# Kernel tuning notes

Hardware: AMD Instinct MI355X
Metric: run time of the kernel (lower is better)

The kernel has to match this reference:

```python
import jax, jax.numpy as jnp
import numpy as np

N_NODES = 50000
N_EDGES = 400000
H, D = 4, 32  # num_heads, per-head dim
NEG_SLOPE = 0.1


def setup_inputs() -> dict:
    key = jax.random.key(0)
    ks = jax.random.split(key, 12)
    inp = {
        'features': jax.random.normal(ks[0], (N_NODES, 256), jnp.float32) * 0.1,
        'src': jax.random.randint(ks[1], (N_EDGES,), 0, N_NODES, jnp.int32),
        'dst': jax.random.randint(ks[2], (N_EDGES,), 0, N_NODES, jnp.int32),
        'w': jax.random.uniform(ks[3], (N_EDGES,), jnp.float32),
        'W1': jax.random.normal(ks[4], (256, 128), jnp.float32) * 0.05,
        'al1': jax.random.normal(ks[5], (H, D), jnp.float32) * 0.1,
        'ar1': jax.random.normal(ks[6], (H, D), jnp.float32) * 0.1,
        'W2': jax.random.normal(ks[7], (128, 128), jnp.float32) * 0.05,
        'al2': jax.random.normal(ks[8], (H, D), jnp.float32) * 0.1,
        'ar2': jax.random.normal(ks[9], (H, D), jnp.float32) * 0.1,
        'Wout': jax.random.normal(ks[10], (256, 128), jnp.float32) * 0.05,
        'bout': jnp.zeros((128,), jnp.float32),
    }
    return inp


def _gat_layer(x, W, al, ar, src, dst, w):
    # x: [N, in_dim] -> ft: [N, H, D]
    ft = (x @ W).reshape(-1, H, D)
    el = jnp.einsum('nhd,hd->nh', ft, al)  # left attention logits per node
    er = jnp.einsum('nhd,hd->nh', ft, ar)
    # edge logits: leaky_relu(el[src] + er[dst]), then edge-weight scaling
    e = jax.nn.leaky_relu(el[src] + er[dst], negative_slope=NEG_SLOPE)  # [E, H]
    e = w[:, None] * e
    # segment softmax over incoming edges of each destination node
    m = jax.ops.segment_max(e, dst, num_segments=N_NODES)  # [N, H]
    a = jnp.exp(e - m[dst])
    s = jax.ops.segment_sum(a, dst, num_segments=N_NODES)
    a = a / s[dst]  # [E, H]
    # weighted scatter-sum aggregation: rst[dst] += a * ft[src]
    msg = ft[src] * a[:, :, None]  # [E, H, D]
    rst = jax.ops.segment_sum(msg, dst, num_segments=N_NODES)  # [N, H, D]
    # activation=relu, then concat heads (contiguous -> reshape)
    return jax.nn.relu(rst).reshape(-1, H * D)


def reference(features, src, dst, w, W1, al1, ar1, W2, al2, ar2, Wout, bout):
    x1 = _gat_layer(features, W1, al1, ar1, src, dst, w)  # [N, 128]
    x2 = _gat_layer(x1, W2, al2, ar2, src, dst, w)        # [N, 128]
    h = jnp.concatenate([x1, x2], axis=-1)                # [N, 256]
    return h @ Wout + bout                                # [N, 128]
```

## Files before the change

kernel.cpp:

```cpp
#include <hip/hip_runtime.h>
#include <math.h>

#define NHEAD 4
#define HDIM 32
#define NEG_SLOPE 0.1f

typedef unsigned short u16;
typedef unsigned int u32;
typedef _Float16 f16;
typedef f16 f16x2 __attribute__((ext_vector_type(2)));
typedef f16 f16x4 __attribute__((ext_vector_type(4)));
typedef f16 f16x8 __attribute__((ext_vector_type(8)));
typedef float f32x4 __attribute__((ext_vector_type(4)));

#define GLLDS16(g, l) __builtin_amdgcn_global_load_lds( \
    (const __attribute__((address_space(1))) void*)(g), \
    (__attribute__((address_space(3))) void*)(l), 16, 0, 0)


__device__ __forceinline__ void cast_panel(const float* __restrict__ W,
                                           const float* __restrict__ al,
                                           const float* __restrict__ ar,
                                           u16* __restrict__ bp, int t, int NC) {
    int per_kt = NC * 16;
    int kt = t / per_kt;
    int rem = t - kt * per_kt;
    int n = rem >> 4;
    int kkp = rem & 15;
    int k = kt * 32 + kkp * 2;
    float v0 = 0.f, v1 = 0.f;
    if (n < 128) {
        v0 = W[(size_t)k * 128 + n];
        v1 = W[(size_t)(k + 1) * 128 + n];
    } else if (n < 136) {
        const float* av = (n < 132) ? al : ar;
        int h = (n < 132) ? (n - 128) : (n - 132);
        float s0 = 0.f, s1 = 0.f;
        for (int d = 0; d < 32; d++) {
            float a = av[h * 32 + d];
            s0 += W[(size_t)k * 128 + h * 32 + d] * a;
            s1 += W[(size_t)(k + 1) * 128 + h * 32 + d] * a;
        }
        v0 = s0; v1 = s1;
    }
    f16x2 p;
    p.x = (f16)v0; p.y = (f16)v1;
    *(f16x2*)&((u32*)bp)[t] = p;
}

__global__ void histcast_k(const int* __restrict__ dst, int* __restrict__ cnt, int E,
                           const float* __restrict__ W1, const float* __restrict__ al1,
                           const float* __restrict__ ar1, u16* __restrict__ b1,
                           const float* __restrict__ W2, const float* __restrict__ al2,
                           const float* __restrict__ ar2, u16* __restrict__ b2,
                           const float* __restrict__ W3, u16* __restrict__ b3) {
    int t = blockIdx.x * 256 + threadIdx.x;
    if (t < E) atomicAdd(&cnt[dst[t]], 1);
    if (t < 18432) cast_panel(W1, al1, ar1, b1, t, 144);
    else if (t < 27648) cast_panel(W2, al2, ar2, b2, t - 18432, 144);
    else if (t < 44032) cast_panel(W3, nullptr, nullptr, b3, t - 27648, 128);
}


__global__ void assign_k(const int* __restrict__ cnt, int* __restrict__ start,
                         int* __restrict__ ctr, int N) {
    __shared__ int s[256];
    __shared__ int base;
    int t = threadIdx.x;
    int i = blockIdx.x * 256 + t;
    int v = (i < N) ? cnt[i] : 0;
    s[t] = v;
    __syncthreads();
    int incl = v;
    for (int off = 1; off < 256; off <<= 1) {
        int add = (t >= off) ? s[t - off] : 0;
        __syncthreads();
        incl += add;
        s[t] = incl;
        __syncthreads();
    }
    if (t == 255) base = atomicAdd(ctr, incl);
    __syncthreads();
    if (i < N) start[i] = base + incl - v;
}

__global__ void scatter_k(const int* __restrict__ src, const int* __restrict__ dst,
                          const float* __restrict__ w, const int* __restrict__ start,
                          int* __restrict__ fill, int2* __restrict__ edge_s, int E) {
    int e = blockIdx.x * 256 + threadIdx.x;
    if (e >= E) return;
    int d = dst[e];
    int p = atomicAdd(&fill[d], 1);
    edge_s[start[d] + p] = make_int2(src[e], __float_as_int(w[e]));
}


template <int NT>
__global__ __launch_bounds__(256) void gemm_h_k(
        const void* __restrict__ Av, int a_is_f16, int lda,
        const u16* __restrict__ Bp,
        const float* __restrict__ bias, float* __restrict__ Cf,
        u16* __restrict__ Ch, float* __restrict__ el, float* __restrict__ er,
        int M, int K) {
    __shared__ u16 As[2048];
    __shared__ u16 Bs[NT * 512];
    int tid = threadIdx.x;
    int w = tid >> 6, lane = tid & 63;
    int row0 = blockIdx.x * 64;
    int mrow = lane & 15;
    int koff = (lane >> 4) * 8;

    f32x4 acc[NT];
#pragma unroll
    for (int nt = 0; nt < NT; nt++) acc[nt] = (f32x4){0.f, 0.f, 0.f, 0.f};

    for (int k0 = 0; k0 < K; k0 += 32) {
        int kt = k0 >> 5;
#pragma unroll
        for (int i = 0; i < (NT * 64 + 255) / 256; i++) {
            int c = tid + i * 256;
            if (c < NT * 64)
                GLLDS16(Bp + (size_t)kt * (NT * 512) + (size_t)c * 8, &Bs[c * 8]);
        }
        if (a_is_f16) {
            const u16* Ah = (const u16*)Av;
            int c = tid;
            int r = c >> 2, kk = (c & 3) << 3;
            GLLDS16(Ah + (size_t)(row0 + r) * lda + k0 + kk, &As[c * 8]);
        } else {
            const float* Af = (const float*)Av;
#pragma unroll
            for (int i = 0; i < 2; i++) {
                int flat = tid + i * 256;
                int r = flat >> 3, c4 = flat & 7;
                int row = min(row0 + r, M - 1);
                float4 v = *(const float4*)&Af[(size_t)row * lda + k0 + c4 * 4];
                f16x4 p;
                p.x = (f16)v.x; p.y = (f16)v.y; p.z = (f16)v.z; p.w = (f16)v.w;
                *(f16x4*)&As[r * 32 + c4 * 4] = p;
            }
        }
        __syncthreads();

        f16x8 ah = *(const f16x8*)&As[(w * 16 + mrow) * 32 + koff];
#pragma unroll
        for (int nt = 0; nt < NT; nt++) {
            f16x8 bh = *(const f16x8*)&Bs[(nt * 16 + mrow) * 32 + koff];
            acc[nt] = __builtin_amdgcn_mfma_f32_16x16x32_f16(ah, bh, acc[nt], 0, 0, 0);
        }
        __syncthreads();
    }

    int rbase = row0 + w * 16 + (lane >> 4) * 4;
#pragma unroll
    for (int nt = 0; nt < 8; nt++) {
        int col = nt * 16 + mrow;
        float bv = bias ? bias[col] : 0.f;
        f32x4 v = acc[nt];
#pragma unroll
        for (int reg = 0; reg < 4; reg++) {
            int rr = rbase + reg;
            if (rr < M) {
                float val = v[reg] + bv;
                if (Cf) Cf[(size_t)rr * 128 + col] = val;
                if (Ch) *(f16*)&Ch[(size_t)rr * 128 + col] = (f16)val;
            }
        }
    }
    if (NT == 9) {
        f32x4 v = acc[8];
#pragma unroll
        for (int reg = 0; reg < 4; reg++) {
            int rr = rbase + reg;
            if (rr < M) {
                if (mrow < 4) el[rr * 4 + mrow] = v[reg];
                else if (mrow < 8) er[rr * 4 + (mrow - 4)] = v[reg];
            }
        }
    }
}


__device__ __forceinline__ float lrelu(float x) {
    return x > 0.f ? x : NEG_SLOPE * x;
}

__global__ __launch_bounds__(256) void agg_k(const u32* __restrict__ fth2,
                                             const float4* __restrict__ el4,
                                             const float4* __restrict__ er4,
                                             const int2* __restrict__ edge_s,
                                             const int* __restrict__ start,
                                             const int* __restrict__ cnt,
                                             u16* __restrict__ xcat,
                                             int ooff, int N) {
    __shared__ float4 sA[256];
    __shared__ int sS[256];
    int wv = threadIdx.x >> 6;
    int n = blockIdx.x * 4 + wv;
    if (n >= N) return;
    int lane = threadIdx.x & 63;
    int head = lane >> 4;
    int r0 = start[n], deg = cnt[n];
    u16* op = &xcat[(size_t)n * 256 + ooff + 2 * lane];
    if (deg == 0) {
        *(u32*)op = 0;
        return;
    }
    float4 ern = er4[n];
    float acc0 = 0.f, acc1 = 0.f;
    if (deg <= 64) {
        float4 a = make_float4(0.f, 0.f, 0.f, 0.f);
        int s = 0;
        if (lane < deg) {
            int2 ep = edge_s[r0 + lane];
            s = ep.x;
            float we = __int_as_float(ep.y);
            float4 e = el4[s];
            a.x = __expf(we * lrelu(e.x + ern.x));
            a.y = __expf(we * lrelu(e.y + ern.y));
            a.z = __expf(we * lrelu(e.z + ern.z));
            a.w = __expf(we * lrelu(e.w + ern.w));
        }
        float4 sm = a;
        for (int m = 1; m < deg; m <<= 1) {
            sm.x += __shfl_xor(sm.x, m);
            sm.y += __shfl_xor(sm.y, m);
            sm.z += __shfl_xor(sm.z, m);
            sm.w += __shfl_xor(sm.w, m);
        }
        a.x = a.x / sm.x; a.y = a.y / sm.y;
        a.z = a.z / sm.z; a.w = a.w / sm.w;
        sA[wv * 64 + lane] = a;
        sS[wv * 64 + lane] = s;
        const float* sAf = (const float*)&sA[wv * 64];
        const int* sSp = &sS[wv * 64];
        int i = 0;
        for (; i + 8 <= deg; i += 8) {
            float wg[8];
            u32 pp[8];
#pragma unroll
            for (int j = 0; j < 8; j++) {
                wg[j] = sAf[(i + j) * 4 + head];
                pp[j] = fth2[(size_t)sSp[i + j] * 64 + lane];
            }
#pragma unroll
            for (int j = 0; j < 8; j++) {
                f16x2 hp = *(const f16x2*)&pp[j];
                acc0 += wg[j] * (float)hp.x;
                acc1 += wg[j] * (float)hp.y;
            }
        }
        for (; i < deg; i++) {
            float wgt = sAf[i * 4 + head];
            u32 p = fth2[(size_t)sSp[i] * 64 + lane];
            f16x2 hp = *(const f16x2*)&p;
            acc0 += wgt * (float)hp.x;
            acc1 += wgt * (float)hp.y;
        }
    } else {
        float4 mx = make_float4(-INFINITY, -INFINITY, -INFINITY, -INFINITY);
        for (int i = lane; i < deg; i += 64) {
            int2 ep = edge_s[r0 + i];
            float we = __int_as_float(ep.y);
            float4 e = el4[ep.x];
            mx.x = fmaxf(mx.x, we * lrelu(e.x + ern.x));
            mx.y = fmaxf(mx.y, we * lrelu(e.y + ern.y));
            mx.z = fmaxf(mx.z, we * lrelu(e.z + ern.z));
            mx.w = fmaxf(mx.w, we * lrelu(e.w + ern.w));
        }
        for (int m = 32; m >= 1; m >>= 1) {
            mx.x = fmaxf(mx.x, __shfl_xor(mx.x, m));
            mx.y = fmaxf(mx.y, __shfl_xor(mx.y, m));
            mx.z = fmaxf(mx.z, __shfl_xor(mx.z, m));
            mx.w = fmaxf(mx.w, __shfl_xor(mx.w, m));
        }
        float4 sm = make_float4(0.f, 0.f, 0.f, 0.f);
        for (int i = lane; i < deg; i += 64) {
            int2 ep = edge_s[r0 + i];
            float we = __int_as_float(ep.y);
            float4 e = el4[ep.x];
            sm.x += __expf(we * lrelu(e.x + ern.x) - mx.x);
            sm.y += __expf(we * lrelu(e.y + ern.y) - mx.y);
            sm.z += __expf(we * lrelu(e.z + ern.z) - mx.z);
            sm.w += __expf(we * lrelu(e.w + ern.w) - mx.w);
        }
        for (int m = 32; m >= 1; m >>= 1) {
            sm.x += __shfl_xor(sm.x, m);
            sm.y += __shfl_xor(sm.y, m);
            sm.z += __shfl_xor(sm.z, m);
            sm.w += __shfl_xor(sm.w, m);
        }
        float4 inv;
        inv.x = 1.f / sm.x; inv.y = 1.f / sm.y;
        inv.z = 1.f / sm.z; inv.w = 1.f / sm.w;
        for (int i = 0; i < deg; i++) {
            int2 ep = edge_s[r0 + i];
            int si = ep.x;
            float we = __int_as_float(ep.y);
            float4 e = el4[si];
            float ax = __expf(we * lrelu(e.x + ern.x) - mx.x) * inv.x;
            float ay = __expf(we * lrelu(e.y + ern.y) - mx.y) * inv.y;
            float az = __expf(we * lrelu(e.z + ern.z) - mx.z) * inv.z;
            float aw = __expf(we * lrelu(e.w + ern.w) - mx.w) * inv.w;
            float wgt = head == 0 ? ax : (head == 1 ? ay : (head == 2 ? az : aw));
            u32 p = fth2[(size_t)si * 64 + lane];
            f16x2 hp = *(const f16x2*)&p;
            acc0 += wgt * (float)hp.x;
            acc1 += wgt * (float)hp.y;
        }
    }
    f16x2 hv;
    hv.x = (f16)fmaxf(acc0, 0.f);
    hv.y = (f16)fmaxf(acc1, 0.f);
    *(f16x2*)op = hv;
}


extern "C" void kernel_launch(void* const* d_in, const int* in_sizes, int n_in,
                              void* d_out, int out_size, void* d_ws, size_t ws_size,
                              hipStream_t stream) {
    const float* features = (const float*)d_in[0];
    const int* src = (const int*)d_in[1];
    const int* dst = (const int*)d_in[2];
    const float* w = (const float*)d_in[3];
    const float* W1 = (const float*)d_in[4];
    const float* al1 = (const float*)d_in[5];
    const float* ar1 = (const float*)d_in[6];
    const float* W2 = (const float*)d_in[7];
    const float* al2 = (const float*)d_in[8];
    const float* ar2 = (const float*)d_in[9];
    const float* Wout = (const float*)d_in[10];
    const float* bout = (const float*)d_in[11];
    float* out = (float*)d_out;

    int N = in_sizes[0] / 256;
    int E = in_sizes[1];
    int Mpad = ((N + 127) / 128) * 128;

    char* ws = (char*)d_ws;
    size_t off = 0;
    auto alloc = [&](size_t bytes) -> void* {
        void* p = ws + off;
        off = (off + bytes + 255) & ~(size_t)255;
        return p;
    };
    size_t Nr = ((size_t)N * 4 + 255) & ~(size_t)255;
    int* cnt = (int*)alloc(2 * Nr + 256);
    int* fill = (int*)((char*)cnt + Nr);
    int* ctr = (int*)((char*)cnt + 2 * Nr);
    int* start = (int*)alloc((size_t)N * 4);
    int2* edge_s = (int2*)alloc((size_t)E * 8);
    u16* fth = (u16*)alloc((size_t)Mpad * 128 * 2);
    float* el = (float*)alloc((size_t)N * 4 * 4);
    float* er = (float*)alloc((size_t)N * 4 * 4);
    u16* xcat = (u16*)alloc((size_t)Mpad * 256 * 2);
    u16* b1 = (u16*)alloc((size_t)18432 * 4);
    u16* b2 = (u16*)alloc((size_t)9216 * 4);
    u16* b3 = (u16*)alloc((size_t)16384 * 4);
    (void)ws_size; (void)n_in; (void)out_size;

    hipMemsetAsync(cnt, 0, 2 * Nr + 256, stream);

    int eb = (E + 255) / 256;
    int nb = (N + 255) / 256;
    int wb = (N + 3) / 4;
    int gb = Mpad / 64;

    histcast_k<<<eb, 256, 0, stream>>>(dst, cnt, E, W1, al1, ar1, b1,
                                       W2, al2, ar2, b2, Wout, b3);
    assign_k<<<nb, 256, 0, stream>>>(cnt, start, ctr, N);
    scatter_k<<<eb, 256, 0, stream>>>(src, dst, w, start, fill, edge_s, E);

    gemm_h_k<9><<<gb, 256, 0, stream>>>(features, 0, 256, b1, nullptr,
                                        nullptr, fth, el, er, N, 256);
    agg_k<<<wb, 256, 0, stream>>>((const u32*)fth, (const float4*)el, (const float4*)er,
                                  edge_s, start, cnt, xcat, 0, N);

    gemm_h_k<9><<<gb, 256, 0, stream>>>(xcat, 1, 256, b2, nullptr,
                                        nullptr, fth, el, er, N, 128);
    agg_k<<<wb, 256, 0, stream>>>((const u32*)fth, (const float4*)el, (const float4*)er,
                                  edge_s, start, cnt, xcat, 128, N);

    gemm_h_k<8><<<gb, 256, 0, stream>>>(xcat, 1, 256, b3, bout,
                                        out, nullptr, nullptr, nullptr, N, 256);
}
```

Baseline: 261.5 us.

## Use MFMA-fragment LDS layout in GEMM and grid-stride aggregation kernel

Reorders the packed weight panel and the A tile in shared memory so each lane's 8-element MFMA fragment is contiguous (lane*8), removing strided LDS reads and likely bank conflicts. The fp32 A path now converts 8 elements per thread with one 16-byte store. The aggregation kernel becomes a grid-stride loop capped at 2048 blocks, and its per-edge normalization uses a fast hardware reciprocal instead of division. Risks are the slightly lower precision of rcp and a possible loss of latency hiding from the capped grid.

```diff
diff --git a/kernel.cpp b/kernel.cpp
--- a/kernel.cpp
+++ b/kernel.cpp
@@ -25,9 +25,13 @@
     int per_kt = NC * 16;
     int kt = t / per_kt;
     int rem = t - kt * per_kt;
-    int n = rem >> 4;
-    int kkp = rem & 15;
-    int k = kt * 32 + kkp * 2;
+    int nt = rem >> 8;
+    int w32 = rem & 255;
+    int kg = w32 >> 6;
+    int col = (w32 >> 2) & 15;
+    int kp = (w32 & 3) * 2;
+    int n = nt * 16 + col;
+    int k = kt * 32 + kg * 8 + kp;
     float v0 = 0.f, v1 = 0.f;
     if (n < 128) {
         v0 = W[(size_t)k * 128 + n];
@@ -108,7 +112,6 @@
     int w = tid >> 6, lane = tid & 63;
     int row0 = blockIdx.x * 64;
     int mrow = lane & 15;
-    int koff = (lane >> 4) * 8;
 
     f32x4 acc[NT];
 #pragma unroll
@@ -125,27 +128,28 @@
         if (a_is_f16) {
             const u16* Ah = (const u16*)Av;
             int c = tid;
-            int r = c >> 2, kk = (c & 3) << 3;
-            GLLDS16(Ah + (size_t)(row0 + r) * lda + k0 + kk, &As[c * 8]);
+            int rblk = c >> 6, kg = (c >> 4) & 3, rr = c & 15;
+            GLLDS16(Ah + (size_t)(row0 + rblk * 16 + rr) * lda + k0 + kg * 8,
+                    &As[c * 8]);
         } else {
             const float* Af = (const float*)Av;
-#pragma unroll
-            for (int i = 0; i < 2; i++) {
-                int flat = tid + i * 256;
-                int r = flat >> 3, c4 = flat & 7;
-                int row = min(row0 + r, M - 1);
-                float4 v = *(const float4*)&Af[(size_t)row * lda + k0 + c4 * 4];
-                f16x4 p;
-                p.x = (f16)v.x; p.y = (f16)v.y; p.z = (f16)v.z; p.w = (f16)v.w;
-                *(f16x4*)&As[r * 32 + c4 * 4] = p;
-            }
+            int c = tid;
+            int rblk = c >> 6, kg = (c >> 4) & 3, rr = c & 15;
+            int row = min(row0 + rblk * 16 + rr, M - 1);
+            const float* ap = &Af[(size_t)row * lda + k0 + kg * 8];
+            float4 v0 = *(const float4*)ap;
+            float4 v1 = *(const float4*)(ap + 4);
+            f16x8 p;
+            p[0] = (f16)v0.x; p[1] = (f16)v0.y; p[2] = (f16)v0.z; p[3] = (f16)v0.w;
+            p[4] = (f16)v1.x; p[5] = (f16)v1.y; p[6] = (f16)v1.z; p[7] = (f16)v1.w;
+            *(f16x8*)&As[c * 8] = p;
         }
         __syncthreads();
 
-        f16x8 ah = *(const f16x8*)&As[(w * 16 + mrow) * 32 + koff];
+        f16x8 ah = *(const f16x8*)&As[w * 512 + lane * 8];
 #pragma unroll
         for (int nt = 0; nt < NT; nt++) {
-            f16x8 bh = *(const f16x8*)&Bs[(nt * 16 + mrow) * 32 + koff];
+            f16x8 bh = *(const f16x8*)&Bs[nt * 512 + lane * 8];
             acc[nt] = __builtin_amdgcn_mfma_f32_16x16x32_f16(ah, bh, acc[nt], 0, 0, 0);
         }
         __syncthreads();
@@ -192,127 +196,131 @@
                                              const int* __restrict__ start,
                                              const int* __restrict__ cnt,
                                              u16* __restrict__ xcat,
-                                             int ooff, int N) {
+                                             int ooff, int N, int ngroups) {
     __shared__ float4 sA[256];
     __shared__ int sS[256];
     int wv = threadIdx.x >> 6;
-    int n = blockIdx.x * 4 + wv;
-    if (n >= N) return;
     int lane = threadIdx.x & 63;
     int head = lane >> 4;
-    int r0 = start[n], deg = cnt[n];
-    u16* op = &xcat[(size_t)n * 256 + ooff + 2 * lane];
-    if (deg == 0) {
-        *(u32*)op = 0;
-        return;
-    }
-    float4 ern = er4[n];
-    float acc0 = 0.f, acc1 = 0.f;
-    if (deg <= 64) {
-        float4 a = make_float4(0.f, 0.f, 0.f, 0.f);
-        int s = 0;
-        if (lane < deg) {
-            int2 ep = edge_s[r0 + lane];
-            s = ep.x;
-            float we = __int_as_float(ep.y);
-            float4 e = el4[s];
-            a.x = __expf(we * lrelu(e.x + ern.x));
-            a.y = __expf(we * lrelu(e.y + ern.y));
-            a.z = __expf(we * lrelu(e.z + ern.z));
-            a.w = __expf(we * lrelu(e.w + ern.w));
-        }
-        float4 sm = a;
-        for (int m = 1; m < deg; m <<= 1) {
-            sm.x += __shfl_xor(sm.x, m);
-            sm.y += __shfl_xor(sm.y, m);
-            sm.z += __shfl_xor(sm.z, m);
-            sm.w += __shfl_xor(sm.w, m);
-        }
-        a.x = a.x / sm.x; a.y = a.y / sm.y;
-        a.z = a.z / sm.z; a.w = a.w / sm.w;
-        sA[wv * 64 + lane] = a;
-        sS[wv * 64 + lane] = s;
-        const float* sAf = (const float*)&sA[wv * 64];
-        const int* sSp = &sS[wv * 64];
-        int i = 0;
-        for (; i + 8 <= deg; i += 8) {
-            float wg[8];
-            u32 pp[8];
-#pragma unroll
-            for (int j = 0; j < 8; j++) {
-                wg[j] = sAf[(i + j) * 4 + head];
-                pp[j] = fth2[(size_t)sSp[i + j] * 64 + lane];
-            }
-#pragma unroll
-            for (int j = 0; j < 8; j++) {
-                f16x2 hp = *(const f16x2*)&pp[j];
-                acc0 += wg[j] * (float)hp.x;
-                acc1 += wg[j] * (float)hp.y;
-            }
-        }
-        for (; i < deg; i++) {
-            float wgt = sAf[i * 4 + head];
-            u32 p = fth2[(size_t)sSp[i] * 64 + lane];
-            f16x2 hp = *(const f16x2*)&p;
-            acc0 += wgt * (float)hp.x;
-            acc1 += wgt * (float)hp.y;
-        }
-    } else {
-        float4 mx = make_float4(-INFINITY, -INFINITY, -INFINITY, -INFINITY);
-        for (int i = lane; i < deg; i += 64) {
-            int2 ep = edge_s[r0 + i];
-            float we = __int_as_float(ep.y);
-            float4 e = el4[ep.x];
-            mx.x = fmaxf(mx.x, we * lrelu(e.x + ern.x));
-            mx.y = fmaxf(mx.y, we * lrelu(e.y + ern.y));
-            mx.z = fmaxf(mx.z, we * lrelu(e.z + ern.z));
-            mx.w = fmaxf(mx.w, we * lrelu(e.w + ern.w));
-        }
-        for (int m = 32; m >= 1; m >>= 1) {
-            mx.x = fmaxf(mx.x, __shfl_xor(mx.x, m));
-            mx.y = fmaxf(mx.y, __shfl_xor(mx.y, m));
-            mx.z = fmaxf(mx.z, __shfl_xor(mx.z, m));
-            mx.w = fmaxf(mx.w, __shfl_xor(mx.w, m));
-        }
-        float4 sm = make_float4(0.f, 0.f, 0.f, 0.f);
-        for (int i = lane; i < deg; i += 64) {
-            int2 ep = edge_s[r0 + i];
-            float we = __int_as_float(ep.y);
-            float4 e = el4[ep.x];
-            sm.x += __expf(we * lrelu(e.x + ern.x) - mx.x);
-            sm.y += __expf(we * lrelu(e.y + ern.y) - mx.y);
-            sm.z += __expf(we * lrelu(e.z + ern.z) - mx.z);
-            sm.w += __expf(we * lrelu(e.w + ern.w) - mx.w);
-        }
-        for (int m = 32; m >= 1; m >>= 1) {
-            sm.x += __shfl_xor(sm.x, m);
-            sm.y += __shfl_xor(sm.y, m);
-            sm.z += __shfl_xor(sm.z, m);
-            sm.w += __shfl_xor(sm.w, m);
-        }
-        float4 inv;
-        inv.x = 1.f / sm.x; inv.y = 1.f / sm.y;
-        inv.z = 1.f / sm.z; inv.w = 1.f / sm.w;
-        for (int i = 0; i < deg; i++) {
-            int2 ep = edge_s[r0 + i];
-            int si = ep.x;
-            float we = __int_as_float(ep.y);
-            float4 e = el4[si];
-            float ax = __expf(we * lrelu(e.x + ern.x) - mx.x) * inv.x;
-            float ay = __expf(we * lrelu(e.y + ern.y) - mx.y) * inv.y;
-            float az = __expf(we * lrelu(e.z + ern.z) - mx.z) * inv.z;
-            float aw = __expf(we * lrelu(e.w + ern.w) - mx.w) * inv.w;
-            float wgt = head == 0 ? ax : (head == 1 ? ay : (head == 2 ? az : aw));
-            u32 p = fth2[(size_t)si * 64 + lane];
-            f16x2 hp = *(const f16x2*)&p;
-            acc0 += wgt * (float)hp.x;
-            acc1 += wgt * (float)hp.y;
-        }
-    }
-    f16x2 hv;
-    hv.x = (f16)fmaxf(acc0, 0.f);
-    hv.y = (f16)fmaxf(acc1, 0.f);
-    *(f16x2*)op = hv;
+    for (int g = blockIdx.x; g < ngroups; g += gridDim.x) {
+        int n = g * 4 + wv;
+        if (n >= N) continue;
+        int r0 = start[n], deg = cnt[n];
+        u16* op = &xcat[(size_t)n * 256 + ooff + 2 * lane];
+        if (deg == 0) {
+            *(u32*)op = 0;
+            continue;
+        }
+        float4 ern = er4[n];
+        float acc0 = 0.f, acc1 = 0.f;
+        if (deg <= 64) {
+            float4 a = make_float4(0.f, 0.f, 0.f, 0.f);
+            int s = 0;
+            if (lane < deg) {
+                int2 ep = edge_s[r0 + lane];
+                s = ep.x;
+                float we = __int_as_float(ep.y);
+                float4 e = el4[s];
+                a.x = __expf(we * lrelu(e.x + ern.x));
+                a.y = __expf(we * lrelu(e.y + ern.y));
+                a.z = __expf(we * lrelu(e.z + ern.z));
+                a.w = __expf(we * lrelu(e.w + ern.w));
+            }
+            float4 sm = a;
+            for (int m = 1; m < deg; m <<= 1) {
+                sm.x += __shfl_xor(sm.x, m);
+                sm.y += __shfl_xor(sm.y, m);
+                sm.z += __shfl_xor(sm.z, m);
+                sm.w += __shfl_xor(sm.w, m);
+            }
+            a.x *= __builtin_amdgcn_rcpf(sm.x);
+            a.y *= __builtin_amdgcn_rcpf(sm.y);
+            a.z *= __builtin_amdgcn_rcpf(sm.z);
+            a.w *= __builtin_amdgcn_rcpf(sm.w);
+            sA[wv * 64 + lane] = a;
+            sS[wv * 64 + lane] = s;
+            const float* sAf = (const float*)&sA[wv * 64];
+            const int* sSp = &sS[wv * 64];
+            int i = 0;
+            for (; i + 8 <= deg; i += 8) {
+                float wg[8];
+                u32 pp[8];
+#pragma unroll
+                for (int j = 0; j < 8; j++) {
+                    wg[j] = sAf[(i + j) * 4 + head];
+                    pp[j] = fth2[(size_t)sSp[i + j] * 64 + lane];
+                }
+#pragma unroll
+                for (int j = 0; j < 8; j++) {
+                    f16x2 hp = *(const f16x2*)&pp[j];
+                    acc0 += wg[j] * (float)hp.x;
+                    acc1 += wg[j] * (float)hp.y;
+                }
+            }
+            for (; i < deg; i++) {
+                float wgt = sAf[i * 4 + head];
+                u32 p = fth2[(size_t)sSp[i] * 64 + lane];
+                f16x2 hp = *(const f16x2*)&p;
+                acc0 += wgt * (float)hp.x;
+                acc1 += wgt * (float)hp.y;
+            }
+        } else {
+            float4 mx = make_float4(-INFINITY, -INFINITY, -INFINITY, -INFINITY);
+            for (int i = lane; i < deg; i += 64) {
+                int2 ep = edge_s[r0 + i];
+                float we = __int_as_float(ep.y);
+                float4 e = el4[ep.x];
+                mx.x = fmaxf(mx.x, we * lrelu(e.x + ern.x));
+                mx.y = fmaxf(mx.y, we * lrelu(e.y + ern.y));
+                mx.z = fmaxf(mx.z, we * lrelu(e.z + ern.z));
+                mx.w = fmaxf(mx.w, we * lrelu(e.w + ern.w));
+            }
+            for (int m = 32; m >= 1; m >>= 1) {
+                mx.x = fmaxf(mx.x, __shfl_xor(mx.x, m));
+                mx.y = fmaxf(mx.y, __shfl_xor(mx.y, m));
+                mx.z = fmaxf(mx.z, __shfl_xor(mx.z, m));
+                mx.w = fmaxf(mx.w, __shfl_xor(mx.w, m));
+            }
+            float4 sm = make_float4(0.f, 0.f, 0.f, 0.f);
+            for (int i = lane; i < deg; i += 64) {
+                int2 ep = edge_s[r0 + i];
+                float we = __int_as_float(ep.y);
+                float4 e = el4[ep.x];
+                sm.x += __expf(we * lrelu(e.x + ern.x) - mx.x);
+                sm.y += __expf(we * lrelu(e.y + ern.y) - mx.y);
+                sm.z += __expf(we * lrelu(e.z + ern.z) - mx.z);
+                sm.w += __expf(we * lrelu(e.w + ern.w) - mx.w);
+            }
+            for (int m = 32; m >= 1; m >>= 1) {
+                sm.x += __shfl_xor(sm.x, m);
+                sm.y += __shfl_xor(sm.y, m);
+                sm.z += __shfl_xor(sm.z, m);
+                sm.w += __shfl_xor(sm.w, m);
+            }
+            float4 inv;
+            inv.x = 1.f / sm.x; inv.y = 1.f / sm.y;
+            inv.z = 1.f / sm.z; inv.w = 1.f / sm.w;
+            for (int i = 0; i < deg; i++) {
+                int2 ep = edge_s[r0 + i];
+                int si = ep.x;
+                float we = __int_as_float(ep.y);
+                float4 e = el4[si];
+                float ax = __expf(we * lrelu(e.x + ern.x) - mx.x) * inv.x;
+                float ay = __expf(we * lrelu(e.y + ern.y) - mx.y) * inv.y;
+                float az = __expf(we * lrelu(e.z + ern.z) - mx.z) * inv.z;
+                float aw = __expf(we * lrelu(e.w + ern.w) - mx.w) * inv.w;
+                float wgt = head == 0 ? ax : (head == 1 ? ay : (head == 2 ? az : aw));
+                u32 p = fth2[(size_t)si * 64 + lane];
+                f16x2 hp = *(const f16x2*)&p;
+                acc0 += wgt * (float)hp.x;
+                acc1 += wgt * (float)hp.y;
+            }
+        }
+        f16x2 hv;
+        hv.x = (f16)fmaxf(acc0, 0.f);
+        hv.y = (f16)fmaxf(acc1, 0.f);
+        *(f16x2*)op = hv;
+    }
 }
 
 
@@ -363,7 +371,8 @@
 
     int eb = (E + 255) / 256;
     int nb = (N + 255) / 256;
-    int wb = (N + 3) / 4;
+    int ng = (N + 3) / 4;
+    int ab = ng < 2048 ? ng : 2048;
     int gb = Mpad / 64;
 
     histcast_k<<<eb, 256, 0, stream>>>(dst, cnt, E, W1, al1, ar1, b1,
@@ -373,13 +382,13 @@
 
     gemm_h_k<9><<<gb, 256, 0, stream>>>(features, 0, 256, b1, nullptr,
                                         nullptr, fth, el, er, N, 256);
-    agg_k<<<wb, 256, 0, stream>>>((const u32*)fth, (const float4*)el, (const float4*)er,
-                                  edge_s, start, cnt, xcat, 0, N);
+    agg_k<<<ab, 256, 0, stream>>>((const u32*)fth, (const float4*)el, (const float4*)er,
+                                  edge_s, start, cnt, xcat, 0, N, ng);
 
     gemm_h_k<9><<<gb, 256, 0, stream>>>(xcat, 1, 256, b2, nullptr,
                                         nullptr, fth, el, er, N, 128);
-    agg_k<<<wb, 256, 0, stream>>>((const u32*)fth, (const float4*)el, (const float4*)er,
-                                  edge_s, start, cnt, xcat, 128, N);
+    agg_k<<<ab, 256, 0, stream>>>((const u32*)fth, (const float4*)el, (const float4*)er,
+                                  edge_s, start, cnt, xcat, 128, N, ng);
 
     gemm_h_k<8><<<gb, 256, 0, stream>>>(xcat, 1, 256, b3, bout,
                                         out, nullptr, nullptr, nullptr, N, 256);
```

After: 258.7 us. Within noise of the previous version (-1.1%).
